# Kernel tuning notes

Hardware: AMD Instinct MI355X
Metric: run time of the kernel (lower is better)

The kernel has to match this reference:

```python
import jax, jax.numpy as jnp
import numpy as np

B, S, D = 4, 8192, 1024
H = 16
HD = D // H          # 64
AD = 64              # approx_dim
EPS = 1e-6


def setup_inputs() -> dict:
    key = jax.random.key(0)
    ks = jax.random.split(key, 5)
    x = jax.random.normal(ks[0], (B, S, D), dtype=jnp.float32)
    # qkv_proj: Linear(D, 3*D)
    W_qkv = jax.random.normal(ks[1], (3 * D, D), dtype=jnp.float32) * (1.0 / np.sqrt(D))
    b_qkv = jnp.zeros((3 * D,), dtype=jnp.float32)
    # proj: Linear(HD, AD) with xavier_uniform init, zero bias
    limit = np.sqrt(6.0 / (HD + AD))
    W_p = jax.random.uniform(ks[2], (AD, HD), dtype=jnp.float32, minval=-limit, maxval=limit)
    b_p = jnp.zeros((AD,), dtype=jnp.float32)
    return {"x": x, "W_qkv": W_qkv, "b_qkv": b_qkv, "W_p": W_p, "b_p": b_p}


def reference(x, W_qkv, b_qkv, W_p, b_p):
    # qkv projection and split
    qkv = x @ W_qkv.T + b_qkv                      # [B,S,3D]
    Q, K, V = jnp.split(qkv, 3, axis=-1)
    # [B,S,D] -> [B,H,S,HD]
    def to_heads(t):
        return t.reshape(B, S, H, HD).transpose(0, 2, 1, 3)
    Q, K, V = to_heads(Q), to_heads(K), to_heads(V)
    # shared projection to approx dim, feature map phi(u) = sqrt(1 + u^2)
    pQ = jnp.einsum('bhsd,ad->bhsa', Q, W_p) + b_p
    pK = jnp.einsum('bhsd,ad->bhsa', K, W_p) + b_p
    phi_Q = jnp.sqrt(1.0 + pQ * pQ)                # [B,H,S,AD]
    phi_K = jnp.sqrt(1.0 + pK * pK)
    # linear attention: O(S) chained contractions
    KTV = jnp.einsum('bhsa,bhsv->bhav', phi_K, V)  # [B,H,AD,HD]
    numerator = jnp.einsum('bhsa,bhav->bhsv', phi_Q, KTV)  # [B,H,S,HD]
    k_sum = phi_K.sum(axis=2)                      # [B,H,AD]
    denominator = jnp.einsum('bhsa,bha->bhs', phi_Q, k_sum)  # [B,H,S]
    head_out = numerator / (denominator[..., None] + EPS)
    # [B,H,S,HD] -> [B,S,D]
    return head_out.transpose(0, 2, 1, 3).reshape(B, S, D)
```

## Files before the change

kernel.cpp:

```cpp
#include <hip/hip_runtime.h>
#include <hip/hip_bf16.h>
#include <cstdint>

static constexpr int Bc  = 4;
static constexpr int Sc  = 8192;
static constexpr int Dc  = 1024;
static constexpr int Hc  = 16;
static constexpr int BHc = Bc * Hc;
static constexpr int Mc  = Bc * Sc;
static constexpr int N3c = 3 * Dc;
static constexpr float EPSc = 1e-6f;

using bf16x8 = __attribute__((ext_vector_type(8))) __bf16;
using f32x4  = __attribute__((ext_vector_type(4))) float;

__device__ __forceinline__ ushort f2bf(float f) {
  union { float f; uint32_t u; } v; v.f = f;
  uint32_t u = v.u;
  return (ushort)((u + 0x7fffu + ((u >> 16) & 1u)) >> 16);
}
__device__ __forceinline__ float bf2f(ushort h) {
  union { uint32_t u; float f; } v; v.u = ((uint32_t)h) << 16;
  return v.f;
}

typedef const __attribute__((address_space(1))) unsigned int* gas_u32p;
typedef __attribute__((address_space(3))) unsigned int* las_u32p;
__device__ __forceinline__ void gld_lds16(const void* g, void* l) {
  __builtin_amdgcn_global_load_lds((gas_u32p)g, (las_u32p)l, 16, 0, 0);
}

__global__ __launch_bounds__(256) void cvt_bf16_k(const float* __restrict__ src,
                                                  ushort* __restrict__ dst, int n4) {
  int i = blockIdx.x * 256 + threadIdx.x;
  if (i < n4) {
    float4 v = reinterpret_cast<const float4*>(src)[i];
    ushort4 o; o.x = f2bf(v.x); o.y = f2bf(v.y); o.z = f2bf(v.z); o.w = f2bf(v.w);
    reinterpret_cast<ushort4*>(dst)[i] = o;
  }
}

__global__ __launch_bounds__(256) void fold_k(const float* __restrict__ Wq,
                                              const float* __restrict__ Wp,
                                              const float* __restrict__ bq,
                                              const float* __restrict__ bp,
                                              ushort* __restrict__ W3b,
                                              float* __restrict__ bias3) {
  const int bx = blockIdx.x;
  const int p = bx >> 4, h = bx & 15;
  const int t = threadIdx.x;
  if (p == 2) {
    const int base = 2048 + h * 64;
    for (int li = t; li < 64 * 256; li += 256) {
      int r = li >> 8, c4 = (li & 255) * 4;
      float4 v = *reinterpret_cast<const float4*>(&Wq[(size_t)(base + r) * 1024 + c4]);
      ushort4 o; o.x = f2bf(v.x); o.y = f2bf(v.y); o.z = f2bf(v.z); o.w = f2bf(v.w);
      *reinterpret_cast<ushort4*>(&W3b[(size_t)(base + r) * 1024 + c4]) = o;
    }
    if (t < 64) bias3[base + t] = bq[base + t];
    return;
  }
  __shared__ ushort Ws[64 * 64];
  __shared__ ushort Tq[256 * 64];
  const int rbase = p * 1024 + h * 64;
  for (int li = t; li < 64 * 16; li += 256) {
    int a = li >> 4, h4 = (li & 15) * 4;
    float4 v = *reinterpret_cast<const float4*>(&Wp[a * 64 + h4]);
    ushort4 o; o.x = f2bf(v.x); o.y = f2bf(v.y); o.z = f2bf(v.z); o.w = f2bf(v.w);
    *reinterpret_cast<ushort4*>(&Ws[a * 64 + h4]) = o;
  }
  if (t < 64) {
    float s = bp[t];
    for (int hd = 0; hd < 64; ++hd) s += Wp[t * 64 + hd] * bq[rbase + hd];
    bias3[rbase + t] = s;
  }
  const int w = t >> 6, lane = t & 63, lr = lane & 15, kg = lane >> 4;
  for (int dt = 0; dt < 4; ++dt) {
    __syncthreads();
    for (int li = t; li < 64 * 64; li += 256) {
      int hd = li >> 6, d4 = (li & 63) * 4;
      float4 v = *reinterpret_cast<const float4*>(&Wq[(size_t)(rbase + hd) * 1024 + dt * 256 + d4]);
      Tq[(d4 + 0) * 64 + hd] = f2bf(v.x);
      Tq[(d4 + 1) * 64 + hd] = f2bf(v.y);
      Tq[(d4 + 2) * 64 + hd] = f2bf(v.z);
      Tq[(d4 + 3) * 64 + hd] = f2bf(v.w);
    }
    __syncthreads();
    f32x4 acc[4][4];
#pragma unroll
    for (int i = 0; i < 4; i++)
#pragma unroll
      for (int j = 0; j < 4; j++) acc[i][j] = (f32x4){0.f, 0.f, 0.f, 0.f};
#pragma unroll
    for (int kk = 0; kk < 2; ++kk) {
      bf16x8 af[4], bfr[4];
#pragma unroll
      for (int i = 0; i < 4; i++)
        af[i] = *reinterpret_cast<const bf16x8*>(&Ws[(i * 16 + lr) * 64 + kk * 32 + kg * 8]);
#pragma unroll
      for (int j = 0; j < 4; j++)
        bfr[j] = *reinterpret_cast<const bf16x8*>(&Tq[(w * 64 + j * 16 + lr) * 64 + kk * 32 + kg * 8]);
#pragma unroll
      for (int i = 0; i < 4; i++)
#pragma unroll
        for (int j = 0; j < 4; j++)
          acc[i][j] = __builtin_amdgcn_mfma_f32_16x16x32_bf16(af[i], bfr[j], acc[i][j], 0, 0, 0);
    }
#pragma unroll
    for (int i = 0; i < 4; i++)
#pragma unroll
      for (int j = 0; j < 4; j++)
#pragma unroll
        for (int r = 0; r < 4; r++)
          W3b[(size_t)(rbase + i * 16 + kg * 4 + r) * 1024 + dt * 256 + w * 64 + j * 16 + lr] =
              f2bf(acc[i][j][r]);
  }
}

__global__ __launch_bounds__(512, 2) void gemm_pipe_k(const ushort* __restrict__ xb,
                                                      const ushort* __restrict__ W3b,
                                                      const float* __restrict__ bias3,
                                                      ushort* __restrict__ Qb,
                                                      ushort* __restrict__ KTb,
                                                      ushort* __restrict__ VTb) {
  __shared__ __align__(16) ushort As[3 * 8192];
  __shared__ __align__(16) ushort Bs[3 * 8192];
  const int t = threadIdx.x, wave = t >> 6, lane = t & 63;
  const int lr = lane & 15, kg = lane >> 4;
  const int wr = wave >> 2, wc = wave & 3;

  const int flat = blockIdx.x;
  const int swz  = (flat & 7) * 192 + (flat >> 3);
  const int n0 = (swz % 12) * 256;
  const int m0 = (swz / 12) * 256;

  const int srow = t >> 2;
  const int sc   = (t & 3) ^ ((t >> 2) & 3) ^ ((t >> 4) & 3);
  const int wb   = (t >> 6) * 512;

  auto STAGE = [&](int tile, int buf) {
    const int kt = tile * 32;
#pragma unroll
    for (int is = 0; is < 2; ++is) {
      gld_lds16(xb  + (size_t)(m0 + is * 128 + srow) * 1024 + kt + sc * 8,
                As + buf * 8192 + is * 4096 + wb);
      gld_lds16(W3b + (size_t)(n0 + is * 128 + srow) * 1024 + kt + sc * 8,
                Bs + buf * 8192 + is * 4096 + wb);
    }
  };

  f32x4 acc[8][4];
#pragma unroll
  for (int f = 0; f < 8; f++)
#pragma unroll
    for (int j = 0; j < 4; j++) acc[f][j] = (f32x4){0.f, 0.f, 0.f, 0.f};

  const int swr = (lr & 3) ^ ((lr >> 2) & 3);
  const int cA  = (kg ^ swr) * 8;
  const ushort* Ard = As + (wr * 128 + lr) * 32 + cA;
  const ushort* Brd = Bs + (wc * 64 + lr) * 32 + cA;

  auto COMPUTE = [&](int buf) {
    bf16x8 af[8], bfr[4];
    const ushort* Ab = Ard + buf * 8192;
    const ushort* Bb = Brd + buf * 8192;
#pragma unroll
    for (int f = 0; f < 8; f++) af[f] = *reinterpret_cast<const bf16x8*>(Ab + f * 512);
#pragma unroll
    for (int j = 0; j < 4; j++) bfr[j] = *reinterpret_cast<const bf16x8*>(Bb + j * 512);
    __builtin_amdgcn_s_setprio(1);
#pragma unroll
    for (int f = 0; f < 8; f++)
#pragma unroll
      for (int j = 0; j < 4; j++)
        acc[f][j] = __builtin_amdgcn_mfma_f32_16x16x32_bf16(af[f], bfr[j], acc[f][j], 0, 0, 0);
    __builtin_amdgcn_s_setprio(0);
  };

  STAGE(0, 0);
  STAGE(1, 1);
  asm volatile("s_waitcnt vmcnt(4)" ::: "memory");
  __builtin_amdgcn_s_barrier();

  int bt = 0, bn = 1, b2 = 2;
#pragma unroll 3
  for (int tile = 0; tile < 30; ++tile) {
    STAGE(tile + 2, b2);
    COMPUTE(bt);
    asm volatile("s_waitcnt vmcnt(4)" ::: "memory");
    __builtin_amdgcn_s_barrier();
    int tmp = bt; bt = bn; bn = b2; b2 = tmp;
  }
  COMPUTE(0);
  asm volatile("s_waitcnt vmcnt(0)" ::: "memory");
  __builtin_amdgcn_s_barrier();
  COMPUTE(1);

  const int n0w  = n0 + wc * 64;
  const int part = n0w >> 10;
  const int h    = (n0w & 1023) >> 6;
  const int bq   = m0 >> 13;
  const int s_base = (m0 & 8191) + wr * 128;
  float bias[4];
#pragma unroll
  for (int j = 0; j < 4; j++) bias[j] = bias3[n0w + j * 16 + lr];

  if (part == 0) {
    ushort* dst = Qb + ((size_t)(bq * Hc + h)) * Sc * 64;
#pragma unroll
    for (int f = 0; f < 8; f++)
#pragma unroll
      for (int j = 0; j < 4; j++)
#pragma unroll
        for (int r = 0; r < 4; r++) {
          float p = acc[f][j][r] + bias[j];
          dst[(size_t)(s_base + f * 16 + kg * 4 + r) * 64 + j * 16 + lr] =
              f2bf(sqrtf(1.f + p * p));
        }
  } else {
    ushort* dst = ((part == 1) ? KTb : VTb) + ((size_t)(bq * Hc + h)) * 64 * Sc;
#pragma unroll
    for (int f = 0; f < 8; f++) {
      const int s = s_base + f * 16 + kg * 4;
#pragma unroll
      for (int j = 0; j < 4; j++) {
        ushort4 o;
        if (part == 1) {
#pragma unroll
          for (int r = 0; r < 4; r++) {
            float p = acc[f][j][r] + bias[j];
            (&o.x)[r] = f2bf(sqrtf(1.f + p * p));
          }
        } else {
#pragma unroll
          for (int r = 0; r < 4; r++) (&o.x)[r] = f2bf(acc[f][j][r] + bias[j]);
        }
        *reinterpret_cast<ushort4*>(&dst[(size_t)(j * 16 + lr) * Sc + s]) = o;
      }
    }
  }
}

__global__ __launch_bounds__(256) void ktv_part_k(const ushort* __restrict__ KT,
                                                  const ushort* __restrict__ VT,
                                                  float* __restrict__ KTVp,
                                                  float* __restrict__ ksump) {
  __shared__ __align__(16) ushort Ks[64 * 128];
  __shared__ __align__(16) ushort Vs[64 * 128];
  __shared__ float red[64][65];
  const int t = threadIdx.x, chunk = blockIdx.x, bh = blockIdx.y;
  const int wave = t >> 6, lane = t & 63, lr = lane & 15, kg = lane >> 4;
  const size_t hb = (size_t)bh * 64 * Sc;
  const int s0 = chunk * 1024;

  f32x4 acc[4][4];
#pragma unroll
  for (int i = 0; i < 4; i++)
#pragma unroll
    for (int j = 0; j < 4; j++) acc[i][j] = (f32x4){0.f, 0.f, 0.f, 0.f};
  float ks_acc = 0.f;

  const int srl = t >> 4;
  const int scc = (t & 15) ^ ((t >> 4) & 7);
  const int wb  = (t >> 6) * 512;
  const int cR = ((wave * 4 + kg) ^ (lr & 7)) * 8;

  for (int st = 0; st < 8; ++st) {
    const int sb = s0 + st * 128;
    __syncthreads();
#pragma unroll
    for (int is = 0; is < 4; ++is) {
      const int row = is * 16 + srl;
      gld_lds16(KT + hb + (size_t)row * Sc + sb + scc * 8, Ks + is * 2048 + wb);
      gld_lds16(VT + hb + (size_t)row * Sc + sb + scc * 8, Vs + is * 2048 + wb);
    }
    __syncthreads();
    {
      bf16x8 af[4], bfr[4];
#pragma unroll
      for (int i = 0; i < 4; i++)
        af[i] = *reinterpret_cast<const bf16x8*>(&Ks[(i * 16 + lr) * 128 + cR]);
#pragma unroll
      for (int j = 0; j < 4; j++)
        bfr[j] = *reinterpret_cast<const bf16x8*>(&Vs[(j * 16 + lr) * 128 + cR]);
#pragma unroll
      for (int i = 0; i < 4; i++)
#pragma unroll
        for (int j = 0; j < 4; j++)
          acc[i][j] = __builtin_amdgcn_mfma_f32_16x16x32_bf16(af[i], bfr[j], acc[i][j], 0, 0, 0);
    }
    if (t < 64) {
      float s = 0.f;
      for (int e = 0; e < 128; e++) s += bf2f(Ks[t * 128 + e]);
      ks_acc += s;
    }
  }

  __syncthreads();
  for (int li = t; li < 64 * 65; li += 256) (&red[0][0])[li] = 0.f;
  __syncthreads();
  for (int w = 0; w < 4; w++) {
    if (wave == w) {
#pragma unroll
      for (int i = 0; i < 4; i++)
#pragma unroll
        for (int j = 0; j < 4; j++)
#pragma unroll
          for (int r = 0; r < 4; r++)
            red[i * 16 + kg * 4 + r][j * 16 + lr] += acc[i][j][r];
    }
    __syncthreads();
  }
  float* outp = KTVp + ((size_t)bh * 8 + chunk) * 4096;
  for (int li = t; li < 4096; li += 256) outp[li] = red[li >> 6][li & 63];
  if (t < 64) ksump[((size_t)bh * 8 + chunk) * 64 + t] = ks_acc;
}

__global__ __launch_bounds__(256) void ktv_red_k(const float* __restrict__ KTVp,
                                                 const float* __restrict__ ksump,
                                                 float* __restrict__ KTV,
                                                 float* __restrict__ ksum) {
  const int bh = blockIdx.x, t = threadIdx.x;
  for (int li = t; li < 4096; li += 256) {
    float s = 0.f;
    for (int c = 0; c < 8; c++) s += KTVp[((size_t)bh * 8 + c) * 4096 + li];
    KTV[(size_t)bh * 4096 + li] = s;
  }
  if (t < 64) {
    float s = 0.f;
    for (int c = 0; c < 8; c++) s += ksump[((size_t)bh * 8 + c) * 64 + t];
    ksum[bh * 64 + t] = s;
  }
}

__global__ __launch_bounds__(256) void out_k(const ushort* __restrict__ Qphi,
                                             const float* __restrict__ KTV,
                                             const float* __restrict__ ksum,
                                             float* __restrict__ out) {
  __shared__ ushort Qs[256][72];
  __shared__ ushort BT[64][72];
  __shared__ float  den[256];
  __shared__ float  kss[64];
  const int t = threadIdx.x;
  const int bh = blockIdx.y, s0 = blockIdx.x * 256;
  const ushort* qb = Qphi + (size_t)bh * Sc * 64 + (size_t)s0 * 64;

#pragma unroll
  for (int i = 0; i < 8; i++) {
    int li = i * 256 + t;
    int r = li >> 3, c8 = li & 7;
    *reinterpret_cast<uint4*>(&Qs[r][c8 * 8]) = *reinterpret_cast<const uint4*>(&qb[li * 8]);
  }
  for (int li = t; li < 4096; li += 256) {
    int a = li >> 6, v = li & 63;
    BT[v][a] = f2bf(KTV[(size_t)bh * 4096 + li]);
  }
  if (t < 64) kss[t] = ksum[bh * 64 + t];
  __syncthreads();

  {
    float d = 0.f;
    for (int a = 0; a < 64; a++) d += bf2f(Qs[t][a]) * kss[a];
    den[t] = d + EPSc;
  }
  __syncthreads();

  const int wave = t >> 6, lane = t & 63, lr = lane & 15, kg = lane >> 4;
  f32x4 acc[4][4];
#pragma unroll
  for (int i = 0; i < 4; i++)
#pragma unroll
    for (int j = 0; j < 4; j++) acc[i][j] = (f32x4){0.f, 0.f, 0.f, 0.f};

#pragma unroll
  for (int ks = 0; ks < 64; ks += 32) {
    bf16x8 af[4], bfr[4];
#pragma unroll
    for (int i = 0; i < 4; i++)
      af[i] = *reinterpret_cast<const bf16x8*>(&Qs[wave * 64 + i * 16 + lr][ks + kg * 8]);
#pragma unroll
    for (int j = 0; j < 4; j++)
      bfr[j] = *reinterpret_cast<const bf16x8*>(&BT[j * 16 + lr][ks + kg * 8]);
#pragma unroll
    for (int i = 0; i < 4; i++)
#pragma unroll
      for (int j = 0; j < 4; j++)
        acc[i][j] = __builtin_amdgcn_mfma_f32_16x16x32_bf16(af[i], bfr[j], acc[i][j], 0, 0, 0);
  }

  const int bq = bh >> 4, h = bh & 15;
#pragma unroll
  for (int i = 0; i < 4; i++) {
#pragma unroll
    for (int j = 0; j < 4; j++) {
#pragma unroll
      for (int r = 0; r < 4; r++) {
        int row = wave * 64 + i * 16 + kg * 4 + r;
        int s = s0 + row;
        int v = j * 16 + lr;
        out[((size_t)bq * Sc + s) * 1024 + h * 64 + v] = acc[i][j][r] / den[row];
      }
    }
  }
}

extern "C" void kernel_launch(void* const* d_in, const int* in_sizes, int n_in,
                              void* d_out, int out_size, void* d_ws, size_t ws_size,
                              hipStream_t stream) {
  const float* x     = (const float*)d_in[0];
  const float* W_qkv = (const float*)d_in[1];
  const float* b_qkv = (const float*)d_in[2];
  const float* W_p   = (const float*)d_in[3];
  const float* b_p   = (const float*)d_in[4];
  float* out = (float*)d_out;

  size_t off = 0;
  auto carve = [&](size_t bytes) -> void* {
    void* p = (char*)d_ws + off;
    off += (bytes + 255) & ~(size_t)255;
    return p;
  };
  const size_t headElems = (size_t)BHc * Sc * 64;
  ushort* xb    = (ushort*)carve((size_t)Mc * Dc * 2);
  ushort* Qb    = (ushort*)carve(headElems * 2);
  ushort* KTb   = (ushort*)carve(headElems * 2);
  ushort* VTb   = (ushort*)carve(headElems * 2);
  ushort* W3b   = (ushort*)carve((size_t)N3c * Dc * 2);
  float*  bias3 = (float*)carve((size_t)N3c * 4);
  float*  KTVp  = (float*)carve((size_t)BHc * 8 * 4096 * 4);
  float*  ksmp  = (float*)carve((size_t)BHc * 8 * 64 * 4);
  float*  KTV   = (float*)carve((size_t)BHc * 4096 * 4);
  float*  ksum  = (float*)carve((size_t)BHc * 64 * 4);
  (void)ws_size; (void)n_in; (void)in_sizes; (void)out_size;

  cvt_bf16_k<<<Mc * Dc / 4 / 256, 256, 0, stream>>>(x, xb, Mc * Dc / 4);
  fold_k<<<48, 256, 0, stream>>>(W_qkv, W_p, b_qkv, b_p, W3b, bias3);
  gemm_pipe_k<<<(Mc / 256) * (N3c / 256), 512, 0, stream>>>(xb, W3b, bias3, Qb, KTb, VTb);
  ktv_part_k<<<dim3(8, BHc), 256, 0, stream>>>(KTb, VTb, KTVp, ksmp);
  ktv_red_k<<<BHc, 256, 0, stream>>>(KTVp, ksmp, KTV, ksum);
  out_k<<<dim3(Sc / 256, BHc), 256, 0, stream>>>(Qb, KTV, ksum, out);
}
```

Before: 429.6 us.

## Deepen QKV GEMM LDS pipeline to four stages with new swizzle

The bf16 QKV GEMM now uses four LDS buffers instead of three. It prefetches three K-tiles ahead in a fully unrolled four-buffer loop, which should better hide global-to-LDS load latency. The LDS XOR swizzle is changed to a row-pair based pattern to cut bank conflicts on the MFMA fragment reads. The fp32-to-bf16 conversion kernel becomes grid-stride with a fixed 2048-block grid. The deeper pipeline raises LDS use to 128 KB per block, which limits occupancy.

```diff
diff --git a/kernel.cpp b/kernel.cpp
--- a/kernel.cpp
+++ b/kernel.cpp
@@ -32,8 +32,7 @@
 
 __global__ __launch_bounds__(256) void cvt_bf16_k(const float* __restrict__ src,
                                                   ushort* __restrict__ dst, int n4) {
-  int i = blockIdx.x * 256 + threadIdx.x;
-  if (i < n4) {
+  for (int i = blockIdx.x * 256 + threadIdx.x; i < n4; i += gridDim.x * 256) {
     float4 v = reinterpret_cast<const float4*>(src)[i];
     ushort4 o; o.x = f2bf(v.x); o.y = f2bf(v.y); o.z = f2bf(v.z); o.w = f2bf(v.w);
     reinterpret_cast<ushort4*>(dst)[i] = o;
@@ -123,8 +122,8 @@
                                                       ushort* __restrict__ Qb,
                                                       ushort* __restrict__ KTb,
                                                       ushort* __restrict__ VTb) {
-  __shared__ __align__(16) ushort As[3 * 8192];
-  __shared__ __align__(16) ushort Bs[3 * 8192];
+  __shared__ __align__(16) ushort As[4 * 8192];
+  __shared__ __align__(16) ushort Bs[4 * 8192];
   const int t = threadIdx.x, wave = t >> 6, lane = t & 63;
   const int lr = lane & 15, kg = lane >> 4;
   const int wr = wave >> 2, wc = wave & 3;
@@ -135,17 +134,17 @@
   const int m0 = (swz / 12) * 256;
 
   const int srow = t >> 2;
-  const int sc   = (t & 3) ^ ((t >> 2) & 3) ^ ((t >> 4) & 3);
-  const int wb   = (t >> 6) * 512;
+  const int sg   = (t & 3) ^ ((t >> 3) & 3);
+  const int swb  = wave * 512;
 
   auto STAGE = [&](int tile, int buf) {
     const int kt = tile * 32;
 #pragma unroll
     for (int is = 0; is < 2; ++is) {
-      gld_lds16(xb  + (size_t)(m0 + is * 128 + srow) * 1024 + kt + sc * 8,
-                As + buf * 8192 + is * 4096 + wb);
-      gld_lds16(W3b + (size_t)(n0 + is * 128 + srow) * 1024 + kt + sc * 8,
-                Bs + buf * 8192 + is * 4096 + wb);
+      gld_lds16(xb  + (size_t)(m0 + is * 128 + srow) * 1024 + kt + sg * 8,
+                As + buf * 8192 + is * 4096 + swb);
+      gld_lds16(W3b + (size_t)(n0 + is * 128 + srow) * 1024 + kt + sg * 8,
+                Bs + buf * 8192 + is * 4096 + swb);
     }
   };
 
@@ -155,10 +154,9 @@
 #pragma unroll
     for (int j = 0; j < 4; j++) acc[f][j] = (f32x4){0.f, 0.f, 0.f, 0.f};
 
-  const int swr = (lr & 3) ^ ((lr >> 2) & 3);
-  const int cA  = (kg ^ swr) * 8;
-  const ushort* Ard = As + (wr * 128 + lr) * 32 + cA;
-  const ushort* Brd = Bs + (wc * 64 + lr) * 32 + cA;
+  const int cp = (kg ^ ((lr >> 1) & 3)) * 8;
+  const ushort* Ard = As + (wr * 128 + lr) * 32 + cp;
+  const ushort* Brd = Bs + (wc * 64 + lr) * 32 + cp;
 
   auto COMPUTE = [&](int buf) {
     bf16x8 af[8], bfr[4];
@@ -179,22 +177,32 @@
 
   STAGE(0, 0);
   STAGE(1, 1);
+  STAGE(2, 2);
+  asm volatile("s_waitcnt vmcnt(8)" ::: "memory");
+  __builtin_amdgcn_s_barrier();
+
+#pragma unroll 1
+  for (int i = 0; i < 7; ++i) {
+    const int tb = i * 4;
+#pragma unroll
+    for (int j = 0; j < 4; ++j) {
+      STAGE(tb + j + 3, (j + 3) & 3);
+      COMPUTE(j);
+      asm volatile("s_waitcnt vmcnt(8)" ::: "memory");
+      __builtin_amdgcn_s_barrier();
+    }
+  }
+  STAGE(31, 3);
+  COMPUTE(0);
+  asm volatile("s_waitcnt vmcnt(8)" ::: "memory");
+  __builtin_amdgcn_s_barrier();
+  COMPUTE(1);
   asm volatile("s_waitcnt vmcnt(4)" ::: "memory");
   __builtin_amdgcn_s_barrier();
-
-  int bt = 0, bn = 1, b2 = 2;
-#pragma unroll 3
-  for (int tile = 0; tile < 30; ++tile) {
-    STAGE(tile + 2, b2);
-    COMPUTE(bt);
-    asm volatile("s_waitcnt vmcnt(4)" ::: "memory");
-    __builtin_amdgcn_s_barrier();
-    int tmp = bt; bt = bn; bn = b2; b2 = tmp;
-  }
-  COMPUTE(0);
+  COMPUTE(2);
   asm volatile("s_waitcnt vmcnt(0)" ::: "memory");
   __builtin_amdgcn_s_barrier();
-  COMPUTE(1);
+  COMPUTE(3);
 
   const int n0w  = n0 + wc * 64;
   const int part = n0w >> 10;
@@ -433,7 +441,7 @@
   float*  ksum  = (float*)carve((size_t)BHc * 64 * 4);
   (void)ws_size; (void)n_in; (void)in_sizes; (void)out_size;
 
-  cvt_bf16_k<<<Mc * Dc / 4 / 256, 256, 0, stream>>>(x, xb, Mc * Dc / 4);
+  cvt_bf16_k<<<2048, 256, 0, stream>>>(x, xb, Mc * Dc / 4);
   fold_k<<<48, 256, 0, stream>>>(W_qkv, W_p, b_qkv, b_p, W3b, bias3);
   gemm_pipe_k<<<(Mc / 256) * (N3c / 256), 512, 0, stream>>>(xb, W3b, bias3, Qb, KTb, VTb);
   ktv_part_k<<<dim3(8, BHc), 256, 0, stream>>>(KTb, VTb, KTVp, ksmp);
```

Result: faster. 417.5 us (-2.8%).
